# Performance work log

Measured on AMD Instinct MI355X. Metric: run time of the kernel, lower is better.

## Reference

```python
import jax, jax.numpy as jnp
import numpy as np

NUM_TAGS = 64
SEQ_LEN = 512
BATCH = 512


def setup_inputs() -> dict:
    key = jax.random.key(0)
    k1, k2, k3, k4, k5 = jax.random.split(key, 5)
    emissions = jax.random.normal(k1, (SEQ_LEN, BATCH, NUM_TAGS), dtype=jnp.float32)
    tags = jax.random.randint(k2, (SEQ_LEN, BATCH), 0, NUM_TAGS, dtype=jnp.int32)
    mask = jnp.ones((SEQ_LEN, BATCH), dtype=jnp.int32)
    start_transitions = jax.random.uniform(k3, (NUM_TAGS,), dtype=jnp.float32)
    end_transitions = jax.random.uniform(k4, (NUM_TAGS,), dtype=jnp.float32)
    transitions = jax.random.uniform(k5, (NUM_TAGS, NUM_TAGS), dtype=jnp.float32)
    return {
        "emissions": emissions,
        "tags": tags,
        "mask": mask,
        "start_transitions": start_transitions,
        "end_transitions": end_transitions,
        "transitions": transitions,
    }


def _compute_score(emissions, tags, mask, start_transitions, end_transitions, transitions):
    # emissions: (S,B,T), tags/mask: (S,B)
    seq_length, batch_size = tags.shape
    maskf = mask.astype(jnp.float32)
    barange = jnp.arange(batch_size)
    # emission scores for gold tags at every step: (S,B)
    emit = jnp.take_along_axis(emissions, tags[:, :, None], axis=2)[:, :, 0]
    # transition scores between consecutive gold tags: (S-1,B)
    trans = transitions[tags[:-1], tags[1:]]
    score = start_transitions[tags[0]] + emit[0]
    score = score + ((trans + emit[1:]) * maskf[1:]).sum(axis=0)
    seq_ends = mask.astype(jnp.int32).sum(axis=0) - 1  # (B,)
    last_tags = tags[seq_ends, barange]
    score = score + end_transitions[last_tags]
    return score  # (B,)


def _compute_normalizer(emissions, mask, start_transitions, end_transitions, transitions):
    # sequential forward-algorithm scan over time
    score0 = start_transitions + emissions[0]  # (B,T)

    def step(score, inp):
        em, m = inp  # em: (B,T), m: (B,)
        # (B,Tprev,Tnext) logsumexp over Tprev
        next_score = jax.nn.logsumexp(
            score[:, :, None] + transitions[None, :, :] + em[:, None, :], axis=1
        )
        score = jnp.where(m[:, None].astype(bool), next_score, score)
        return score, None

    score, _ = jax.lax.scan(step, score0, (emissions[1:], mask[1:]))
    return jax.nn.logsumexp(score + end_transitions, axis=1)  # (B,)


def reference(emissions, tags, mask, start_transitions, end_transitions, transitions):
    numerator = _compute_score(emissions, tags, mask, start_transitions, end_transitions, transitions)
    denominator = _compute_normalizer(emissions, mask, start_transitions, end_transitions, transitions)
    llh = numerator - denominator
    return llh.sum()  # reduction='sum'
```

## Files before the change

kernel.cpp:

```cpp
#include <hip/hip_runtime.h>

#define T   512
#define B   512
#define NT  64
#define QS  16
#define NQ  (T / QS)
#define RING 4

typedef _Float16 h2 __attribute__((ext_vector_type(2)));

__device__ __forceinline__ float rflf(float x) {
    return __uint_as_float(__builtin_amdgcn_readfirstlane(__float_as_uint(x)));
}

__device__ __forceinline__ float dot2(h2 a, h2 b, float c) {
#if __has_builtin(__builtin_amdgcn_fdot2)
    return __builtin_amdgcn_fdot2(a, b, c, false);
#else
    return c + (float)a.x * (float)b.x + (float)a.y * (float)b.y;
#endif
}

__global__ __launch_bounds__(64) void crf_fused(
    const float* __restrict__ emissions,
    const int*   __restrict__ tags,
    const int*   __restrict__ mask,
    const float* __restrict__ startT,
    const float* __restrict__ endT,
    const float* __restrict__ trans,
    float* __restrict__ out)
{
    const int j = threadIdx.x;

    __shared__ __align__(16) float ebuf[RING][QS][NT];

    if (blockIdx.x < B) {
        const int b = blockIdx.x;

        h2 Eh[NT / 2];
#pragma unroll
        for (int m = 0; m < NT / 2; ++m) {
            Eh[m].x = (_Float16)__expf(trans[(2 * m)     * NT + j]);
            Eh[m].y = (_Float16)__expf(trans[(2 * m + 1) * NT + j]);
        }

        const int jr = j >> 4;
        const int c0 = (j & 15) * 4;
        float4 sA[4];

        auto issue_q = [&](int g) {
#pragma unroll
            for (int k = 0; k < 4; ++k) {
                const int t = g * QS + 4 * k + jr;
                sA[k] = *(const float4*)&emissions[((size_t)t * B + b) * NT + c0];
            }
        };
        auto write_q = [&](int g) {
#pragma unroll
            for (int k = 0; k < 4; ++k) {
                float4 w;
                w.x = __expf(sA[k].x); w.y = __expf(sA[k].y);
                w.z = __expf(sA[k].z); w.w = __expf(sA[k].w);
                *(float4*)&ebuf[g & (RING - 1)][4 * k + jr][c0] = w;
            }
        };

        for (int g = 0; g < 3; ++g) { issue_q(g); write_q(g); }
        issue_q(3);

        const float e0  = emissions[(size_t)b * NT + j];
        const float sc0 = startT[j] + e0;
        const float S0  = rflf(sc0);
        float q = __expf(sc0 - S0);
        int   K = 0;

        int pk_i;
        {
            const int qi = __float_as_int(q);
            const int qo = __builtin_amdgcn_update_dpp(0, qi, 0xB1, 0xF, 0xF, true);
            pk_i = __builtin_bit_cast(int,
                    __builtin_amdgcn_cvt_pkrtz(q, __int_as_float(qo)));
        }

        int mpre = mask[j * B + b];
        unsigned long long mbc = 0;

        for (int x = 0; x < NQ; ++x) {
            const int gw = (x + 3 < NQ) ? x + 3 : NQ - 1;
            write_q(gw);
            const int gl = (x + 4 < NQ) ? x + 4 : NQ - 1;
            issue_q(gl);

            if ((x & 3) == 0) {
                mbc = __ballot(mpre != 0);
                const int cn = ((x >> 2) + 1 < 8) ? (x >> 2) + 1 : 7;
                mpre = mask[(cn * 64 + j) * B + b];
            }

            const int tt0 = (x == 0) ? 1 : 0;
#pragma unroll 4
            for (int tt = tt0; tt < QS; ++tt) {
                const float X = ebuf[x & (RING - 1)][tt][j];

                float a0 = 0.f, a1 = 0.f, a2 = 0.f, a3 = 0.f;
#pragma unroll
                for (int n = 0; n < 8; ++n) {
                    const int u0 = __builtin_amdgcn_readlane(pk_i, 8 * n + 0);
                    const int u1 = __builtin_amdgcn_readlane(pk_i, 8 * n + 2);
                    const int u2 = __builtin_amdgcn_readlane(pk_i, 8 * n + 4);
                    const int u3 = __builtin_amdgcn_readlane(pk_i, 8 * n + 6);
                    a0 = dot2(__builtin_bit_cast(h2, u0), Eh[4 * n + 0], a0);
                    a1 = dot2(__builtin_bit_cast(h2, u1), Eh[4 * n + 1], a1);
                    a2 = dot2(__builtin_bit_cast(h2, u2), Eh[4 * n + 2], a2);
                    a3 = dot2(__builtin_bit_cast(h2, u3), Eh[4 * n + 3], a3);
                }
                const float p = (a0 + a1) + (a2 + a3);

                const int bits = __builtin_amdgcn_readfirstlane(__float_as_int(p));
                const int k    = ((bits >> 23) & 255) - 127;
                const float r  = __int_as_float((127 - k) << 23);

                const int  ttc = ((x & 3) << 4) + tt;
                const bool mc  = (mbc >> ttc) & 1ull;
                const float qn = p * r * X;
                q = mc ? qn : q;
                K += mc ? k : 0;

                const int qi = __float_as_int(q);
                const int qo = __builtin_amdgcn_update_dpp(0, qi, 0xB1, 0xF, 0xF, true);
                pk_i = __builtin_bit_cast(int,
                        __builtin_amdgcn_cvt_pkrtz(q, __int_as_float(qo)));
            }
        }

        float v = q * __expf(endT[j]);
#pragma unroll
        for (int off = 32; off > 0; off >>= 1)
            v += __shfl_xor(v, off);
        if (j == 0)
            atomicAdd(out, -(S0 + (float)K * 0.69314718f + __logf(v)));

    } else {
        const int b = blockIdx.x - B;

        float acc = 0.f;
        int   cnt = 0;
#pragma unroll
        for (int m = 0; m < T / 64; ++m) {
            const int t  = j + 64 * m;
            const int mv = mask[t * B + b];
            const int tg = tags[t * B + b];
            cnt += (int)__popcll(__ballot(mv != 0));
            if (t == 0) {
                acc += startT[tg] + emissions[(size_t)b * NT + tg];
            } else if (mv) {
                const int tp = tags[(t - 1) * B + b];
                acc += trans[tp * NT + tg]
                     + emissions[(size_t)(t * B + b) * NT + tg];
            }
        }
#pragma unroll
        for (int off = 32; off > 0; off >>= 1)
            acc += __shfl_xor(acc, off);
        if (j == 0) {
            const int last = tags[(size_t)(cnt - 1) * B + b];
            atomicAdd(out, acc + endT[last]);
        }
    }
}

extern "C" void kernel_launch(void* const* d_in, const int* in_sizes, int n_in,
                              void* d_out, int out_size, void* d_ws, size_t ws_size,
                              hipStream_t stream) {
    const float* emissions = (const float*)d_in[0];
    const int*   tags      = (const int*)  d_in[1];
    const int*   mask      = (const int*)  d_in[2];
    const float* startT    = (const float*)d_in[3];
    const float* endT      = (const float*)d_in[4];
    const float* trans     = (const float*)d_in[5];
    float* out = (float*)d_out;

    hipMemsetAsync(out, 0, sizeof(float), stream);
    crf_fused<<<2 * B, 64, 0, stream>>>(
        emissions, tags, mask, startT, endT, trans, out);
}
```

Measured before the change: 194.6 us.

## Restructure CRF forward recurrence with deferred normalization and mask-free fast path

Peels the first time step and reworks the sequential step so the scale exponent used to normalize q comes from the previous step's sum. This takes the readfirstlane-to-multiply dependency off the critical chain, and the r factor is folded into the emission value early. Each 16-step chunk whose mask bits are all set runs a mask-free step variant, and emission values from LDS are prefetched one step ahead. The loop is now unroll 1 with sched barriers and uses 8 accumulators. The deferred scaling carries a bias of 2 in the exponent to keep values in fp16 range, which risks overflow or underflow if consecutive sums differ widely.

```diff
diff --git a/kernel.cpp b/kernel.cpp
--- a/kernel.cpp
+++ b/kernel.cpp
@@ -20,6 +20,8 @@
     return c + (float)a.x * (float)b.x + (float)a.y * (float)b.y;
 #endif
 }
+
+__device__ __forceinline__ h2 bch2(int u) { return __builtin_bit_cast(h2, u); }
 
 __global__ __launch_bounds__(64) void crf_fused(
     const float* __restrict__ emissions,
@@ -82,8 +84,91 @@
                     __builtin_amdgcn_cvt_pkrtz(q, __int_as_float(qo)));
         }
 
+        float* eflat = &ebuf[0][0][0];
+        int bits_prev;
         int mpre = mask[j * B + b];
         unsigned long long mbc = 0;
+
+        {
+            int u[32];
+#pragma unroll
+            for (int n = 0; n < 32; ++n)
+                u[n] = __builtin_amdgcn_readlane(pk_i, 2 * n);
+            float a[8] = {0.f, 0.f, 0.f, 0.f, 0.f, 0.f, 0.f, 0.f};
+#pragma unroll
+            for (int n = 0; n < 32; ++n)
+                a[n & 7] = dot2(bch2(u[n]), Eh[n], a[n & 7]);
+            const float p = ((a[0] + a[1]) + (a[2] + a[3]))
+                          + ((a[4] + a[5]) + (a[6] + a[7]));
+            bits_prev = __builtin_amdgcn_readfirstlane(__float_as_int(p));
+            const int  k = ((bits_prev >> 23) & 255) - 127;
+            const float r = __int_as_float((125 - k) << 23);
+            const float X1 = eflat[NT + j];
+            const int  m1 = mask[B + b];
+            if (m1) { q = (p * X1) * r; K = k + 2; }
+            const int qo = __builtin_amdgcn_update_dpp(0, __float_as_int(q),
+                                                       0xB1, 0xF, 0xF, true);
+            pk_i = __builtin_bit_cast(int,
+                    __builtin_amdgcn_cvt_pkrtz(q, __int_as_float(qo)));
+        }
+
+        float Xc = eflat[2 * NT + j];
+        float Xn = eflat[3 * NT + j];
+
+        auto stepF = [&](int s) {
+            int u[32];
+#pragma unroll
+            for (int n = 0; n < 32; ++n)
+                u[n] = __builtin_amdgcn_readlane(pk_i, 2 * n);
+            __builtin_amdgcn_sched_barrier(0);
+            const int  k = ((bits_prev >> 23) & 255) - 127;
+            const float r = __int_as_float((125 - k) << 23);
+            K += k + 2;
+            float a[8] = {0.f, 0.f, 0.f, 0.f, 0.f, 0.f, 0.f, 0.f};
+#pragma unroll
+            for (int n = 0; n < 32; ++n)
+                a[n & 7] = dot2(bch2(u[n]), Eh[n], a[n & 7]);
+            const float sXr = Xc * r;
+            const float p = ((a[0] + a[1]) + (a[2] + a[3]))
+                          + ((a[4] + a[5]) + (a[6] + a[7]));
+            q = p * sXr;
+            bits_prev = __builtin_amdgcn_readfirstlane(__float_as_int(p));
+            const int qo = __builtin_amdgcn_update_dpp(0, __float_as_int(q),
+                                                       0xB1, 0xF, 0xF, true);
+            pk_i = __builtin_bit_cast(int,
+                    __builtin_amdgcn_cvt_pkrtz(q, __int_as_float(qo)));
+            Xc = Xn;
+            Xn = eflat[((s + 2) & 63) * NT + j];
+        };
+
+        auto stepM = [&](int s) {
+            int u[32];
+#pragma unroll
+            for (int n = 0; n < 32; ++n)
+                u[n] = __builtin_amdgcn_readlane(pk_i, 2 * n);
+            __builtin_amdgcn_sched_barrier(0);
+            const int  k = ((bits_prev >> 23) & 255) - 127;
+            const float r = __int_as_float((125 - k) << 23);
+            const bool mc = (mbc >> (s & 63)) & 1ull;
+            const float mf = mc ? 1.0f : 0.0f;
+            K += mc ? (k + 2) : 0;
+            float a[8] = {0.f, 0.f, 0.f, 0.f, 0.f, 0.f, 0.f, 0.f};
+#pragma unroll
+            for (int n = 0; n < 32; ++n)
+                a[n & 7] = dot2(bch2(u[n]), Eh[n], a[n & 7]);
+            const float sXr = Xc * r;
+            const float p = ((a[0] + a[1]) + (a[2] + a[3]))
+                          + ((a[4] + a[5]) + (a[6] + a[7]));
+            const float qn = p * sXr;
+            q = fmaf(mf, qn - q, q);
+            bits_prev = __builtin_amdgcn_readfirstlane(__float_as_int(p));
+            const int qo = __builtin_amdgcn_update_dpp(0, __float_as_int(q),
+                                                       0xB1, 0xF, 0xF, true);
+            pk_i = __builtin_bit_cast(int,
+                    __builtin_amdgcn_cvt_pkrtz(q, __int_as_float(qo)));
+            Xc = Xn;
+            Xn = eflat[((s + 2) & 63) * NT + j];
+        };
 
         for (int x = 0; x < NQ; ++x) {
             const int gw = (x + 3 < NQ) ? x + 3 : NQ - 1;
@@ -97,39 +182,15 @@
                 mpre = mask[(cn * 64 + j) * B + b];
             }
 
-            const int tt0 = (x == 0) ? 1 : 0;
-#pragma unroll 4
-            for (int tt = tt0; tt < QS; ++tt) {
-                const float X = ebuf[x & (RING - 1)][tt][j];
-
-                float a0 = 0.f, a1 = 0.f, a2 = 0.f, a3 = 0.f;
-#pragma unroll
-                for (int n = 0; n < 8; ++n) {
-                    const int u0 = __builtin_amdgcn_readlane(pk_i, 8 * n + 0);
-                    const int u1 = __builtin_amdgcn_readlane(pk_i, 8 * n + 2);
-                    const int u2 = __builtin_amdgcn_readlane(pk_i, 8 * n + 4);
-                    const int u3 = __builtin_amdgcn_readlane(pk_i, 8 * n + 6);
-                    a0 = dot2(__builtin_bit_cast(h2, u0), Eh[4 * n + 0], a0);
-                    a1 = dot2(__builtin_bit_cast(h2, u1), Eh[4 * n + 1], a1);
-                    a2 = dot2(__builtin_bit_cast(h2, u2), Eh[4 * n + 2], a2);
-                    a3 = dot2(__builtin_bit_cast(h2, u3), Eh[4 * n + 3], a3);
-                }
-                const float p = (a0 + a1) + (a2 + a3);
-
-                const int bits = __builtin_amdgcn_readfirstlane(__float_as_int(p));
-                const int k    = ((bits >> 23) & 255) - 127;
-                const float r  = __int_as_float((127 - k) << 23);
-
-                const int  ttc = ((x & 3) << 4) + tt;
-                const bool mc  = (mbc >> ttc) & 1ull;
-                const float qn = p * r * X;
-                q = mc ? qn : q;
-                K += mc ? k : 0;
-
-                const int qi = __float_as_int(q);
-                const int qo = __builtin_amdgcn_update_dpp(0, qi, 0xB1, 0xF, 0xF, true);
-                pk_i = __builtin_bit_cast(int,
-                        __builtin_amdgcn_cvt_pkrtz(q, __int_as_float(qo)));
+            const unsigned qb = (unsigned)(mbc >> ((x & 3) << 4)) & 0xFFFFu;
+            const int tt0 = (x == 0) ? 2 : 0;
+
+            if (qb == 0xFFFFu) {
+#pragma unroll 1
+                for (int tt = tt0; tt < QS; ++tt) stepF(x * QS + tt);
+            } else {
+#pragma unroll 1
+                for (int tt = tt0; tt < QS; ++tt) stepM(x * QS + tt);
             }
         }
 
```

New measurement: 193.4 us. About the same (-0.6%).
